# Optimization experiments

Measured on AMD Instinct MI355X. Metric: run time of the kernel, lower is better.

## Reference

```python
import jax, jax.numpy as jnp
import numpy as np

N, E, G = 20000, 160000, 64
IN_FULL, X_START, X_END = 16, 4, 10
H, OUT, RH, NE, K = 512, 512, 128, 4, 2
NL = 3               # GraphConv layers per expert
SPS, STEMP = 0.3, 1.0  # size_prior_strength, size_temperature


def setup_inputs() -> dict:
    key = jax.random.key(0)
    ks = jax.random.split(key, 10)
    def w(k, shape, fan):
        return jax.random.normal(k, shape, jnp.float32) / np.float32(np.sqrt(fan))
    return dict(
        x=jax.random.normal(ks[0], (N, IN_FULL), jnp.float32),
        edge_index=jax.random.randint(ks[1], (2, E), 0, N),
        batch=jnp.sort(jax.random.randint(ks[2], (N,), 0, G)),
        num_graphs=G,
        enc_W1=w(ks[3], (X_END - X_START, H), X_END - X_START), enc_b1=jnp.zeros((H,), jnp.float32),
        enc_W2=w(ks[4], (H, H), H), enc_b2=jnp.zeros((H,), jnp.float32),
        r_W1=w(ks[5], (H + 2, RH), H + 2), r_b1=jnp.zeros((RH,), jnp.float32),
        ln_g=jnp.ones((RH,), jnp.float32), ln_b=jnp.zeros((RH,), jnp.float32),
        r_W2=w(ks[6], (RH, NE), RH), r_b2=jnp.zeros((NE,), jnp.float32),
        size_centers=jnp.linspace(0.0, 1.0, NE).astype(jnp.float32),
        W_rel=w(ks[7], (NE, NL, H, H), H),       # GraphConv lin_rel weights (stacked)
        b_rel=jnp.zeros((NE, NL, H), jnp.float32),
        W_root=w(ks[8], (NE, NL, H, H), H),      # GraphConv lin_root weights (no bias)
    )


def reference(x, edge_index, batch, num_graphs, enc_W1, enc_b1, enc_W2, enc_b2,
              r_W1, r_b1, ln_g, ln_b, r_W2, r_b2, size_centers, W_rel, b_rel, W_root):
    src, dst = edge_index[0], edge_index[1]
    # encoder: Linear -> ReLU -> Linear on sliced node features
    h = jax.nn.relu(x[:, X_START:X_END] @ enc_W1 + enc_b1) @ enc_W2 + enc_b2
    # per-graph size features (log_nodes_edges mode)
    nodes = jnp.maximum(jax.ops.segment_sum(jnp.ones((N,), x.dtype), batch, num_segments=num_graphs), 1.0)
    edges = jax.ops.segment_sum(jnp.ones((E,), x.dtype), batch[src], num_segments=num_graphs)
    log_n, log_e = jnp.log(nodes), jnp.log1p(edges)
    f = jnp.stack([log_n, log_e], axis=-1)
    f = (f - f.mean(0, keepdims=True)) / (f.std(0, keepdims=True) + 1e-6)
    size_norm = (log_n - log_n.min()) / (log_n.max() - log_n.min() + 1e-6)
    # router: Linear -> LayerNorm -> ReLU -> Linear, plus size prior
    r = jnp.concatenate([h, f[batch]], axis=-1) @ r_W1 + r_b1
    r = (r - r.mean(-1, keepdims=True)) / jnp.sqrt(r.var(-1, keepdims=True) + 1e-5) * ln_g + ln_b
    logits = jax.nn.relu(r) @ r_W2 + r_b2
    prior = -(size_norm[batch][:, None] - size_centers[None, :]) ** 2 / STEMP
    logits = (1.0 - SPS) * logits + SPS * prior
    probs = jax.nn.softmax(logits, axis=-1)
    # top-k sparse gating, renormalized
    v, ix = jax.lax.top_k(probs, K)
    v = v / (v.sum(-1, keepdims=True) + 1e-8)
    weights = jnp.zeros_like(probs).at[jnp.arange(N)[:, None], ix].set(v)  # [N, NE]
    # GraphConv: out_i = (sum_{j->i} z_j) @ W_rel + b_rel + z_i @ W_root
    def gconv(z, Wr, br, Wo):
        agg = jax.ops.segment_sum(z[src], dst, num_segments=N)
        return agg @ Wr + br + z @ Wo
    out = jnp.zeros((N, OUT), x.dtype)
    for e in range(NE):  # small fixed expert count
        z = jax.nn.relu(gconv(h, W_rel[e, 0], b_rel[e, 0], W_root[e, 0]))
        z = jax.nn.relu(gconv(z, W_rel[e, 1], b_rel[e, 1], W_root[e, 1]))
        z = gconv(z, W_rel[e, 2], b_rel[e, 2], W_root[e, 2])
        out = out + weights[:, e:e + 1] * z
    return out
```

## Files before the change

kernel.cpp:

```cpp
#include <hip/hip_runtime.h>
#include <math.h>

#define N_NODES 20000
#define N_EDGES 160000
#define G_GRAPHS 64
#define H_DIM 512
#define RH_DIM 128
#define NE_EXP 4
#define P_ROWS 20096
#define EH_BLOCKS 64
#define WSZ (512 * 512)

typedef __attribute__((ext_vector_type(8))) short bf16x8;
typedef __attribute__((ext_vector_type(4))) float f32x4;

__device__ __forceinline__ ushort f2bf(float f) {
    uint u = __float_as_uint(f);
    return (ushort)((u + 0x7FFFu + ((u >> 16) & 1u)) >> 16);
}
__device__ __forceinline__ float bf2f(ushort h) {
    return __uint_as_float(((uint)h) << 16);
}

__device__ __forceinline__ void async_copy16(const void* g, void* l) {
    __builtin_amdgcn_global_load_lds(
        (__attribute__((address_space(1))) void*)g,
        (__attribute__((address_space(3))) void*)l, 16, 0, 0);
}

__device__ __forceinline__ int xcd_swizzle(int orig, int nwg) {
    const int q = nwg >> 3, r = nwg & 7;
    const int xcd = orig & 7, sid = orig >> 3;
    return (xcd < r ? xcd * (q + 1) : r * (q + 1) + (xcd - r) * q) + sid;
}

template<bool RELU, int EPI, int NE2>
__global__ __launch_bounds__(256)
void gemm_grp(const ushort* __restrict__ A1, size_t a1es,
              const ushort* __restrict__ W1, size_t w1es,
              const ushort* __restrict__ A2, size_t a2es,
              const ushort* __restrict__ W2, size_t w2es,
              const float* __restrict__ bias, size_t bes,
              const float* __restrict__ wcol,
              ushort* __restrict__ out0, size_t oes)
{
    __shared__ char smem[32768];
    const int tid = threadIdx.x;
    const int w = tid >> 6, lane = tid & 63;

    const int wgid = xcd_swizzle(blockIdx.x, gridDim.x);
    const int m0 = (wgid / (4 * NE2)) * 128;
    const int rem = wgid % (4 * NE2);
    const int e  = rem % NE2;
    const int n0 = (rem / NE2) * 128;

    const ushort* __restrict__ A1e = A1 + (size_t)e * a1es;
    const ushort* __restrict__ W1e = W1 + (size_t)e * w1es;
    const ushort* __restrict__ A2e = A2 + (size_t)e * a2es;
    const ushort* __restrict__ W2e = W2 + (size_t)e * w2es;
    const float*  __restrict__ be  = bias + (size_t)e * bes;
    ushort* __restrict__ oe = out0 + (size_t)e * oes;

    f32x4 acc[4][4];
#pragma unroll
    for (int i = 0; i < 4; ++i)
#pragma unroll
        for (int j = 0; j < 4; ++j) acc[i][j] = (f32x4){0.f, 0.f, 0.f, 0.f};

    const int srow = lane >> 2, schk = lane & 3;
    const int wr = w >> 1, wc = w & 1;
    const int row16 = lane & 15;
    const uint koffB = (uint)(lane >> 4) * 16u;
    const uint aoff0 = (uint)(wr * 64 + row16) * 64u + koffB;
    const uint boff0 = 8192u + (uint)(wc * 64 + row16) * 64u + koffB;

    auto stage = [&](int buf, int t) {
        const ushort* __restrict__ A  = (t < 16) ? A1e : A2e;
        const ushort* __restrict__ Wt = (t < 16) ? W1e : W2e;
        const int kt = (t & 15) * 32;
        char* base = smem + buf * 16384;
#pragma unroll
        for (int c = 0; c < 2; ++c) {
            const int rb = c * 64 + w * 16;
            async_copy16(A  + (size_t)(m0 + rb + srow) * 512 + kt + schk * 8, base + rb * 64);
            async_copy16(Wt + (size_t)(n0 + rb + srow) * 512 + kt + schk * 8, base + 8192 + rb * 64);
        }
    };
    auto compute = [&](int buf) {
        const char* base = smem + buf * 16384;
        bf16x8 af[4], bfr[4];
#pragma unroll
        for (int i = 0; i < 4; ++i) af[i] = *(const bf16x8*)(base + aoff0 + i * 1024);
#pragma unroll
        for (int j = 0; j < 4; ++j) bfr[j] = *(const bf16x8*)(base + boff0 + j * 1024);
#pragma unroll
        for (int i = 0; i < 4; ++i)
#pragma unroll
            for (int j = 0; j < 4; ++j)
                acc[i][j] = __builtin_amdgcn_mfma_f32_16x16x32_bf16(af[i], bfr[j], acc[i][j], 0, 0, 0);
    };

    stage(0, 0);
    for (int t = 0; t < 31; ++t) {
        stage((t + 1) & 1, t + 1);
        asm volatile("s_waitcnt vmcnt(4)" ::: "memory");
        __builtin_amdgcn_s_barrier();
        compute(t & 1);
        __builtin_amdgcn_s_barrier();
    }
    asm volatile("s_waitcnt vmcnt(0)" ::: "memory");
    __builtin_amdgcn_s_barrier();
    compute(1);

#pragma unroll
    for (int i = 0; i < 4; ++i) {
        const int r0 = m0 + wr * 64 + i * 16 + (lane >> 4) * 4;
#pragma unroll
        for (int j = 0; j < 4; ++j) {
            const int c = n0 + wc * 64 + j * 16 + row16;
            const float bj = be[c];
#pragma unroll
            for (int q2 = 0; q2 < 4; ++q2) {
                const int r = r0 + q2;
                float v = acc[i][j][q2] + bj;
                if (EPI == 0) {
                    if (RELU) v = fmaxf(v, 0.f);
                    oe[(size_t)r * 512 + c] = f2bf(v);
                } else {
                    const float wrow = (r < N_NODES) ? wcol[(size_t)r * 4 + e] : 0.f;
                    oe[(size_t)r * 512 + c] = f2bf(v * wrow);
                }
            }
        }
    }
}

template<int NPASS, int EPI, int NBN>
__global__ __launch_bounds__(256)
void gemm_mfma(const ushort* __restrict__ A0, const ushort* __restrict__ W0,
               const ushort* __restrict__ A1p, const ushort* __restrict__ W1p,
               const ushort* __restrict__ A2p, const ushort* __restrict__ W2p,
               const float* __restrict__ bias,
               void* __restrict__ out0, void* __restrict__ out1, int Ncols)
{
    __shared__ char smem[32768];
    const int tid = threadIdx.x;
    const int w = tid >> 6, lane = tid & 63;

    const int wgid = xcd_swizzle(blockIdx.x, gridDim.x);
    const int m0 = (wgid / NBN) * 128;
    const int n0 = (wgid % NBN) * 128;

    f32x4 acc[4][4];
#pragma unroll
    for (int i = 0; i < 4; ++i)
#pragma unroll
        for (int j = 0; j < 4; ++j) acc[i][j] = (f32x4){0.f, 0.f, 0.f, 0.f};

    const int srow = lane >> 2, schk = lane & 3;
    const int wr = w >> 1, wc = w & 1;
    const int row16 = lane & 15;
    const uint koffB = (uint)(lane >> 4) * 16u;
    const uint aoff0 = (uint)(wr * 64 + row16) * 64u + koffB;
    const uint boff0 = 8192u + (uint)(wc * 64 + row16) * 64u + koffB;

    const int NT = NPASS * 16;
    auto Asel = [&](int t) -> const ushort* { return (t < 16) ? A0 : ((t < 32) ? A1p : A2p); };
    auto Wsel = [&](int t) -> const ushort* { return (t < 16) ? W0 : ((t < 32) ? W1p : W2p); };

    auto stage = [&](int buf, int t) {
        const ushort* __restrict__ A  = Asel(t);
        const ushort* __restrict__ Wt = Wsel(t);
        const int kt = (t & 15) * 32;
        char* base = smem + buf * 16384;
#pragma unroll
        for (int c = 0; c < 2; ++c) {
            const int rb = c * 64 + w * 16;
            async_copy16(A  + (size_t)(m0 + rb + srow) * 512 + kt + schk * 8, base + rb * 64);
            async_copy16(Wt + (size_t)(n0 + rb + srow) * 512 + kt + schk * 8, base + 8192 + rb * 64);
        }
    };
    auto compute = [&](int buf) {
        const char* base = smem + buf * 16384;
        bf16x8 af[4], bfr[4];
#pragma unroll
        for (int i = 0; i < 4; ++i) af[i] = *(const bf16x8*)(base + aoff0 + i * 1024);
#pragma unroll
        for (int j = 0; j < 4; ++j) bfr[j] = *(const bf16x8*)(base + boff0 + j * 1024);
#pragma unroll
        for (int i = 0; i < 4; ++i)
#pragma unroll
            for (int j = 0; j < 4; ++j)
                acc[i][j] = __builtin_amdgcn_mfma_f32_16x16x32_bf16(af[i], bfr[j], acc[i][j], 0, 0, 0);
    };

    stage(0, 0);
    for (int t = 0; t < NT - 1; ++t) {
        stage((t + 1) & 1, t + 1);
        asm volatile("s_waitcnt vmcnt(4)" ::: "memory");
        __builtin_amdgcn_s_barrier();
        compute(t & 1);
        __builtin_amdgcn_s_barrier();
    }
    asm volatile("s_waitcnt vmcnt(0)" ::: "memory");
    __builtin_amdgcn_s_barrier();
    compute((NT - 1) & 1);

#pragma unroll
    for (int i = 0; i < 4; ++i) {
        const int r0 = m0 + wr * 64 + i * 16 + (lane >> 4) * 4;
#pragma unroll
        for (int j = 0; j < 4; ++j) {
            const int c = n0 + wc * 64 + j * 16 + row16;
            const float bj = (EPI == 5) ? 0.f : bias[c];
#pragma unroll
            for (int q2 = 0; q2 < 4; ++q2) {
                const int r = r0 + q2;
                float v = acc[i][j][q2] + bj;
                if (EPI == 4) {
                    const ushort hi = f2bf(v);
                    const ushort lo = f2bf(v - bf2f(hi));
                    ((ushort*)out0)[(size_t)r * Ncols + c] = hi;
                    ((ushort*)out1)[(size_t)r * Ncols + c] = lo;
                } else {
                    ((float*)out0)[(size_t)r * Ncols + c] = v;
                }
            }
        }
    }
}

__global__ __launch_bounds__(256)
void reduce_wz_kernel(const uint* __restrict__ wz4, float2* __restrict__ out)
{
    const size_t idx = (size_t)blockIdx.x * 256 + threadIdx.x;
    const size_t es = (size_t)P_ROWS * 256;
    const uint a = wz4[idx], b = wz4[idx + es];
    const uint c = wz4[idx + 2 * es], d = wz4[idx + 3 * es];
    float lo = bf2f((ushort)(a & 0xffffu)) + bf2f((ushort)(b & 0xffffu))
             + bf2f((ushort)(c & 0xffffu)) + bf2f((ushort)(d & 0xffffu));
    float hi = bf2f((ushort)(a >> 16)) + bf2f((ushort)(b >> 16))
             + bf2f((ushort)(c >> 16)) + bf2f((ushort)(d >> 16));
    out[idx] = make_float2(lo, hi);
}

__global__ void encoder1_kernel(const float* __restrict__ x, const float* __restrict__ W1,
                                const float* __restrict__ b1,
                                ushort* __restrict__ t1hi, ushort* __restrict__ t1lo)
{
    const int idx = blockIdx.x * blockDim.x + threadIdx.x;
    if (idx >= P_ROWS * H_DIM) return;
    const int i = idx / H_DIM, j = idx - i * H_DIM;
    float v = 0.f;
    if (i < N_NODES) {
        const float* xr = &x[i * 16 + 4];
        v = b1[j];
#pragma unroll
        for (int k = 0; k < 6; ++k) v = fmaf(xr[k], W1[k * H_DIM + j], v);
        v = fmaxf(v, 0.f);
    }
    const ushort hi = f2bf(v);
    t1hi[idx] = hi;
    t1lo[idx] = f2bf(v - bf2f(hi));
}

__global__ void zero_ints_kernel(int* __restrict__ p, int n)
{
    const int idx = blockIdx.x * blockDim.x + threadIdx.x;
    if (idx < n) p[idx] = 0;
}

__global__ void graph_bounds_kernel(const int* __restrict__ batch, int* __restrict__ gstart)
{
    const int g = threadIdx.x;
    if (g > G_GRAPHS) return;
    int lo = 0, hi = N_NODES;
    while (lo < hi) {
        const int mid = (lo + hi) >> 1;
        if (batch[mid] < g) lo = mid + 1; else hi = mid;
    }
    gstart[g] = lo;
}

__global__ __launch_bounds__(256)
void edge_hist_kernel(const int* __restrict__ src, const int* __restrict__ dst,
                      const int* __restrict__ batch,
                      int* __restrict__ part, int* __restrict__ deg)
{
    __shared__ int hist[G_GRAPHS];
    const int tid = threadIdx.x;
    if (tid < G_GRAPHS) hist[tid] = 0;
    __syncthreads();
    for (int e = blockIdx.x * 256 + tid; e < N_EDGES; e += EH_BLOCKS * 256) {
        atomicAdd(&deg[dst[e]], 1);
        atomicAdd(&hist[batch[src[e]]], 1);
    }
    __syncthreads();
    if (tid < G_GRAPHS) part[blockIdx.x * G_GRAPHS + tid] = hist[tid];
}

__global__ void stats_finalize_kernel(const int* __restrict__ gstart, const int* __restrict__ part,
                                      float* __restrict__ f_norm, float* __restrict__ size_norm)
{
    const int g = threadIdx.x;
    const float nn = fmaxf((float)(gstart[g + 1] - gstart[g]), 1.0f);
    int ec = 0;
#pragma unroll 8
    for (int b = 0; b < EH_BLOCKS; ++b) ec += part[b * G_GRAPHS + g];
    const float ee = (float)ec;
    const float ln = logf(nn);
    const float le = log1pf(ee);
    float s0 = ln, s1 = le;
#pragma unroll
    for (int o = 32; o > 0; o >>= 1) { s0 += __shfl_xor(s0, o); s1 += __shfl_xor(s1, o); }
    const float m0 = s0 / 64.f, m1 = s1 / 64.f;
    const float d0 = ln - m0, d1 = le - m1;
    float v0 = d0 * d0, v1 = d1 * d1;
#pragma unroll
    for (int o = 32; o > 0; o >>= 1) { v0 += __shfl_xor(v0, o); v1 += __shfl_xor(v1, o); }
    const float sd0 = sqrtf(v0 / 64.f), sd1 = sqrtf(v1 / 64.f);
    float mn = ln, mx = ln;
#pragma unroll
    for (int o = 32; o > 0; o >>= 1) {
        mn = fminf(mn, __shfl_xor(mn, o));
        mx = fmaxf(mx, __shfl_xor(mx, o));
    }
    f_norm[g * 2 + 0] = d0 / (sd0 + 1e-6f);
    f_norm[g * 2 + 1] = d1 / (sd1 + 1e-6f);
    size_norm[g] = (ln - mn) / (mx - mn + 1e-6f);
}

__global__ void scan_kernel(const int* __restrict__ in, int* __restrict__ row_ptr,
                            int* __restrict__ cursor, int n)
{
    __shared__ int wsum[16];
    __shared__ int carry_s;
    const int tid = threadIdx.x;
    const int lane = tid & 63, wv = tid >> 6;
    if (tid == 0) carry_s = 0;
    __syncthreads();
    for (int base = 0; base < n; base += 1024) {
        const int idx = base + tid;
        const int v = (idx < n) ? in[idx] : 0;
        int x = v;
#pragma unroll
        for (int o = 1; o < 64; o <<= 1) { const int t = __shfl_up(x, o); if (lane >= o) x += t; }
        if (lane == 63) wsum[wv] = x;
        __syncthreads();
        const int carry = carry_s;
        if (wv == 0) {
            int y = (lane < 16) ? wsum[lane] : 0;
#pragma unroll
            for (int o = 1; o < 16; o <<= 1) { const int t = __shfl_up(y, o); if (lane >= o) y += t; }
            if (lane < 16) wsum[lane] = y;
        }
        __syncthreads();
        const int woff = (wv > 0) ? wsum[wv - 1] : 0;
        const int excl = x - v + woff + carry;
        if (idx < n) { row_ptr[idx] = excl; cursor[idx] = excl; }
        __syncthreads();
        if (tid == 0) carry_s = carry + wsum[15];
        __syncthreads();
    }
    if (tid == 0) row_ptr[n] = carry_s;
}

__global__ void scatter_kernel(const int* __restrict__ src, const int* __restrict__ dst,
                               int* __restrict__ cursor, int* __restrict__ csr_col)
{
    const int e = blockIdx.x * blockDim.x + threadIdx.x;
    if (e >= N_EDGES) return;
    const int d = dst[e];
    const int slot = atomicAdd(&cursor[d], 1);
    csr_col[slot] = src[e];
}

__global__ void sort_adj_kernel(const int* __restrict__ row_ptr, int* __restrict__ csr_col)
{
    const int i = blockIdx.x * blockDim.x + threadIdx.x;
    if (i >= N_NODES) return;
    const int b = row_ptr[i], e = row_ptr[i + 1];
    for (int p = b + 1; p < e; ++p) {
        const int key = csr_col[p];
        int q = p - 1;
        while (q >= b && csr_col[q] > key) { csr_col[q + 1] = csr_col[q]; --q; }
        csr_col[q + 1] = key;
    }
}

__global__ __launch_bounds__(256)
void aggregate_bf16(const uint4* __restrict__ z4, const int* __restrict__ row_ptr,
                    const int* __restrict__ csr_col, uint4* __restrict__ agg4)
{
    const size_t es = (size_t)blockIdx.y * P_ROWS * 64;
    const uint4* __restrict__ zz = z4 + es;
    uint4* __restrict__ aa = agg4 + es;
    const int i = blockIdx.x * 4 + (threadIdx.x >> 6);
    const int lane = threadIdx.x & 63;
    const int b = row_ptr[i], e = row_ptr[i + 1];
    float acc[8];
#pragma unroll
    for (int k = 0; k < 8; ++k) acc[k] = 0.f;
    auto add8 = [&](uint4 v) {
        acc[0] += bf2f((ushort)(v.x & 0xffffu)); acc[1] += bf2f((ushort)(v.x >> 16));
        acc[2] += bf2f((ushort)(v.y & 0xffffu)); acc[3] += bf2f((ushort)(v.y >> 16));
        acc[4] += bf2f((ushort)(v.z & 0xffffu)); acc[5] += bf2f((ushort)(v.z >> 16));
        acc[6] += bf2f((ushort)(v.w & 0xffffu)); acc[7] += bf2f((ushort)(v.w >> 16));
    };
    int p = b;
    for (; p + 2 <= e; p += 2) {
        const uint4 v0 = zz[(size_t)csr_col[p] * 64 + lane];
        const uint4 v1 = zz[(size_t)csr_col[p + 1] * 64 + lane];
        add8(v0);
        add8(v1);
    }
    if (p < e) add8(zz[(size_t)csr_col[p] * 64 + lane]);
    uint4 o;
    o.x = (uint)f2bf(acc[0]) | ((uint)f2bf(acc[1]) << 16);
    o.y = (uint)f2bf(acc[2]) | ((uint)f2bf(acc[3]) << 16);
    o.z = (uint)f2bf(acc[4]) | ((uint)f2bf(acc[5]) << 16);
    o.w = (uint)f2bf(acc[6]) | ((uint)f2bf(acc[7]) << 16);
    aa[(size_t)i * 64 + lane] = o;
}

__global__ __launch_bounds__(256)
void transpose_f32_to_bf16(const float* __restrict__ W, ushort* __restrict__ Wt)
{
    __shared__ float tile[32][33];
    const float* Wm = W + (size_t)blockIdx.z * WSZ;
    ushort* Wtm = Wt + (size_t)blockIdx.z * WSZ;
    const int c0 = blockIdx.x * 32, r0 = blockIdx.y * 32;
    const int tc = threadIdx.x & 31, tr = threadIdx.x >> 5;
#pragma unroll
    for (int it = 0; it < 4; ++it)
        tile[tr + it * 8][tc] = Wm[(size_t)(r0 + tr + it * 8) * 512 + c0 + tc];
    __syncthreads();
#pragma unroll
    for (int it = 0; it < 4; ++it) {
        const int cr = tr + it * 8;
        Wtm[(size_t)(c0 + cr) * 512 + r0 + tc] = f2bf(tile[tc][cr]);
    }
}

__global__ __launch_bounds__(256)
void transpose_split_kernel(const float* __restrict__ W, ushort* __restrict__ Whi,
                            ushort* __restrict__ Wlo, int Nin)
{
    __shared__ float tile[32][33];
    const int c0 = blockIdx.x * 32;
    const int r0 = blockIdx.y * 32;
    const int tc = threadIdx.x & 31, tr = threadIdx.x >> 5;
#pragma unroll
    for (int it = 0; it < 4; ++it)
        tile[tr + it * 8][tc] = W[(size_t)(r0 + tr + it * 8) * Nin + c0 + tc];
    __syncthreads();
#pragma unroll
    for (int it = 0; it < 4; ++it) {
        const int cr = tr + it * 8;
        const float v = tile[tc][cr];
        const ushort hi = f2bf(v);
        Whi[(size_t)(c0 + cr) * 512 + r0 + tc] = hi;
        Wlo[(size_t)(c0 + cr) * 512 + r0 + tc] = f2bf(v - bf2f(hi));
    }
}

__global__ __launch_bounds__(128)
void router_kernel(const float* __restrict__ rtmp, const int* __restrict__ batch,
                   const float* __restrict__ rW1, const float* __restrict__ rb1,
                   const float* __restrict__ lng, const float* __restrict__ lnb,
                   const float* __restrict__ rW2, const float* __restrict__ rb2,
                   const float* __restrict__ centers,
                   const float* __restrict__ f_norm, const float* __restrict__ size_norm,
                   float* __restrict__ weights)
{
    const int i = blockIdx.x;
    const int j = threadIdx.x;
    const int g = batch[i];
    const float f0 = f_norm[g * 2], f1 = f_norm[g * 2 + 1];
    float r = rtmp[(size_t)i * RH_DIM + j]
            + f0 * rW1[512 * RH_DIM + j] + f1 * rW1[513 * RH_DIM + j] + rb1[j];

    __shared__ float part[2];
    __shared__ float rbuf[RH_DIM];
    __shared__ float lbuf[4];
    const int lane = j & 63, wv = j >> 6;

    float s = r;
#pragma unroll
    for (int o = 32; o > 0; o >>= 1) s += __shfl_xor(s, o);
    if (lane == 0) part[wv] = s;
    __syncthreads();
    const float mean = (part[0] + part[1]) / 128.f;
    __syncthreads();
    const float d = r - mean;
    float v = d * d;
#pragma unroll
    for (int o = 32; o > 0; o >>= 1) v += __shfl_xor(v, o);
    if (lane == 0) part[wv] = v;
    __syncthreads();
    const float var = (part[0] + part[1]) / 128.f;
    const float rn = d / sqrtf(var + 1e-5f) * lng[j] + lnb[j];
    rbuf[j] = fmaxf(rn, 0.f);
    __syncthreads();

    if (j < 4) {
        float acc = rb2[j];
        for (int t = 0; t < RH_DIM; ++t) acc = fmaf(rbuf[t], rW2[t * 4 + j], acc);
        const float sn = size_norm[g];
        const float dd = sn - centers[j];
        lbuf[j] = 0.7f * acc + 0.3f * (-(dd * dd));
    }
    __syncthreads();
    if (j == 0) {
        float p[4];
        const float mx = fmaxf(fmaxf(lbuf[0], lbuf[1]), fmaxf(lbuf[2], lbuf[3]));
#pragma unroll
        for (int c = 0; c < 4; ++c) p[c] = expf(lbuf[c] - mx);
        const float ssum = p[0] + p[1] + p[2] + p[3];
#pragma unroll
        for (int c = 0; c < 4; ++c) p[c] /= ssum;
        int i1 = 0;
#pragma unroll
        for (int c = 1; c < 4; ++c) if (p[c] > p[i1]) i1 = c;
        int i2 = -1;
#pragma unroll
        for (int c = 0; c < 4; ++c) {
            if (c == i1) continue;
            if (i2 < 0 || p[c] > p[i2]) i2 = c;
        }
        const float vs = p[i1] + p[i2] + 1e-8f;
        float wout[4] = {0.f, 0.f, 0.f, 0.f};
        wout[i1] = p[i1] / vs;
        wout[i2] = p[i2] / vs;
#pragma unroll
        for (int c = 0; c < 4; ++c) weights[(size_t)i * 4 + c] = wout[c];
    }
}

extern "C" void kernel_launch(void* const* d_in, const int* in_sizes, int n_in,
                              void* d_out, int out_size, void* d_ws, size_t ws_size,
                              hipStream_t stream)
{
    const float* x       = (const float*)d_in[0];
    const int*   ei      = (const int*)d_in[1];
    const int*   batch   = (const int*)d_in[2];
    const float* enc_W1  = (const float*)d_in[4];
    const float* enc_b1  = (const float*)d_in[5];
    const float* enc_W2  = (const float*)d_in[6];
    const float* enc_b2  = (const float*)d_in[7];
    const float* r_W1    = (const float*)d_in[8];
    const float* r_b1    = (const float*)d_in[9];
    const float* ln_g    = (const float*)d_in[10];
    const float* ln_b    = (const float*)d_in[11];
    const float* r_W2    = (const float*)d_in[12];
    const float* r_b2    = (const float*)d_in[13];
    const float* centers = (const float*)d_in[14];
    const float* W_rel   = (const float*)d_in[15];
    const float* b_rel   = (const float*)d_in[16];
    const float* W_root  = (const float*)d_in[17];
    const int* src = ei;
    const int* dst = ei + N_EDGES;
    float* out = (float*)d_out;

    const size_t PF = (size_t)P_ROWS * H_DIM;
    const size_t PF2 = PF * 2;
    const int mode = (ws_size >= (size_t)375 * 1024 * 1024) ? 2
                   : (ws_size >= (size_t)295 * 1024 * 1024) ? 1 : 0;
    const int zaW = (mode >= 1) ? 4 : 2;
    const int zbW = (mode == 2) ? 4 : 2;

    char* wsp = (char*)d_ws;
    size_t off = 0;
    auto alloc = [&](size_t bytes) -> char* {
        char* p = wsp + off;
        off = (off + bytes + 255) & ~(size_t)255;
        return p;
    };
    char* region1 = alloc(PF * 4);
    ushort* t1hi = (ushort*)region1;
    ushort* t1lo = (ushort*)(region1 + PF * 2);
    ushort* wz4  = (ushort*)region1;
    char* region2 = alloc(PF * 4);
    ushort* h_hi = (ushort*)region2;
    ushort* h_lo = (ushort*)(region2 + PF * 2);
    char* B_zA = alloc(PF2 * zaW);
    ushort* zAe = (ushort*)B_zA;
    float*  rtmp = (float*)B_zA;
    char* B_zB = alloc(PF2 * zbW);
    ushort* zBe = (ushort*)B_zB;
    char* B_ag = alloc(PF2 * zbW);
    ushort* agge = (ushort*)B_ag;
    ushort* aggH16 = (ushort*)alloc(PF * 2);
    ushort* Wt_rel16  = (ushort*)alloc((size_t)12 * WSZ * 2);
    ushort* Wt_root16 = (ushort*)alloc((size_t)12 * WSZ * 2);
    ushort* W2t_hi = (ushort*)alloc((size_t)WSZ * 2);
    ushort* W2t_lo = (ushort*)alloc((size_t)WSZ * 2);
    ushort* rW1t_hi = (ushort*)alloc((size_t)128 * 512 * 2);
    ushort* rW1t_lo = (ushort*)alloc((size_t)128 * 512 * 2);
    float*  weights = (float*)alloc((size_t)P_ROWS * 4 * 4);
    int* deg     = (int*)alloc((size_t)N_NODES * 4);
    int* gstart  = (int*)alloc((size_t)(G_GRAPHS + 1) * 4);
    int* part    = (int*)alloc((size_t)EH_BLOCKS * G_GRAPHS * 4);
    int* row_ptr = (int*)alloc((size_t)(N_NODES + 1) * 4);
    int* cursor  = (int*)alloc((size_t)N_NODES * 4);
    int* csr_col = (int*)alloc((size_t)N_EDGES * 4);
    float* f_norm    = (float*)alloc((size_t)G_GRAPHS * 2 * 4);
    float* size_norm = (float*)alloc((size_t)G_GRAPHS * 4);
    (void)in_sizes; (void)n_in; (void)out_size;

    const int enc_nwg  = 4 * (P_ROWS / 128);
    const int rtr_nwg  = 1 * (P_ROWS / 128);
    const int grp_nwg2 = 8 * (P_ROWS / 128);
    const int grp_nwg4 = 16 * (P_ROWS / 128);
    const dim3 tr_grid(16, 16, 12);
    const dim3 agg_grid1(N_NODES / 4, 1);
    const dim3 agg_grid2(N_NODES / 4, 2);
    const dim3 agg_grid4(N_NODES / 4, 4);

    zero_ints_kernel<<<(N_NODES + 255) / 256, 256, 0, stream>>>(deg, N_NODES);
    transpose_f32_to_bf16<<<tr_grid, 256, 0, stream>>>(W_rel, Wt_rel16);
    transpose_f32_to_bf16<<<tr_grid, 256, 0, stream>>>(W_root, Wt_root16);
    transpose_split_kernel<<<dim3(16, 16), 256, 0, stream>>>(enc_W2, W2t_hi, W2t_lo, 512);
    transpose_split_kernel<<<dim3(4, 16), 256, 0, stream>>>(r_W1, rW1t_hi, rW1t_lo, 128);
    graph_bounds_kernel<<<1, 128, 0, stream>>>(batch, gstart);
    edge_hist_kernel<<<EH_BLOCKS, 256, 0, stream>>>(src, dst, batch, part, deg);
    stats_finalize_kernel<<<1, 64, 0, stream>>>(gstart, part, f_norm, size_norm);
    encoder1_kernel<<<(P_ROWS * H_DIM + 255) / 256, 256, 0, stream>>>(x, enc_W1, enc_b1, t1hi, t1lo);
    gemm_mfma<3, 4, 4><<<enc_nwg, 256, 0, stream>>>(
        t1hi, W2t_hi, t1hi, W2t_lo, t1lo, W2t_hi, enc_b2, h_hi, h_lo, 512);
    gemm_mfma<3, 5, 1><<<rtr_nwg, 256, 0, stream>>>(
        h_hi, rW1t_hi, h_hi, rW1t_lo, h_lo, rW1t_hi, nullptr, rtmp, nullptr, 128);
    router_kernel<<<N_NODES, 128, 0, stream>>>(rtmp, batch, r_W1, r_b1, ln_g, ln_b,
                                               r_W2, r_b2, centers, f_norm, size_norm, weights);
    scan_kernel<<<1, 1024, 0, stream>>>(deg, row_ptr, cursor, N_NODES);
    scatter_kernel<<<(N_EDGES + 255) / 256, 256, 0, stream>>>(src, dst, cursor, csr_col);
    sort_adj_kernel<<<(N_NODES + 255) / 256, 256, 0, stream>>>(row_ptr, csr_col);
    aggregate_bf16<<<agg_grid1, 256, 0, stream>>>((const uint4*)h_hi, row_ptr, csr_col,
                                                  (uint4*)aggH16);

    const size_t WES = (size_t)3 * WSZ;
    const size_t BES = (size_t)3 * 512;
    if (mode == 2) {
        gemm_grp<true, 0, 4><<<grp_nwg4, 256, 0, stream>>>(
            aggH16, 0, Wt_rel16, WES, h_hi, 0, Wt_root16, WES, b_rel, BES, nullptr, zAe, PF);
        aggregate_bf16<<<agg_grid4, 256, 0, stream>>>((const uint4*)zAe, row_ptr, csr_col,
                                                      (uint4*)agge);
        gemm_grp<true, 0, 4><<<grp_nwg4, 256, 0, stream>>>(
            agge, PF, Wt_rel16 + WSZ, WES, zAe, PF, Wt_root16 + WSZ, WES, b_rel + 512, BES,
            nullptr, zBe, PF);
        aggregate_bf16<<<agg_grid4, 256, 0, stream>>>((const uint4*)zBe, row_ptr, csr_col,
                                                      (uint4*)agge);
        gemm_grp<false, 6, 4><<<grp_nwg4, 256, 0, stream>>>(
            agge, PF, Wt_rel16 + 2 * WSZ, WES, zBe, PF, Wt_root16 + 2 * WSZ, WES, b_rel + 1024, BES,
            weights, wz4, PF);
    } else if (mode == 1) {
        gemm_grp<true, 0, 4><<<grp_nwg4, 256, 0, stream>>>(
            aggH16, 0, Wt_rel16, WES, h_hi, 0, Wt_root16, WES, b_rel, BES, nullptr, zAe, PF);
        for (int p = 0; p < 2; ++p) {
            const size_t eb = (size_t)(p * 2);
            const ushort* WrP = Wt_rel16  + eb * WES;
            const ushort* WoP = Wt_root16 + eb * WES;
            const float*  brP = b_rel + eb * BES;
            const ushort* zAp = zAe + eb * PF;
            ushort* wzP = wz4 + eb * PF;
            aggregate_bf16<<<agg_grid2, 256, 0, stream>>>((const uint4*)zAp, row_ptr, csr_col,
                                                          (uint4*)agge);
            gemm_grp<true, 0, 2><<<grp_nwg2, 256, 0, stream>>>(
                agge, PF, WrP + WSZ, WES, zAp, PF, WoP + WSZ, WES, brP + 512, BES, nullptr, zBe, PF);
            aggregate_bf16<<<agg_grid2, 256, 0, stream>>>((const uint4*)zBe, row_ptr, csr_col,
                                                          (uint4*)agge);
            gemm_grp<false, 6, 2><<<grp_nwg2, 256, 0, stream>>>(
                agge, PF, WrP + 2 * WSZ, WES, zBe, PF, WoP + 2 * WSZ, WES, brP + 1024, BES,
                weights + eb, wzP, PF);
        }
    } else {
        for (int p = 0; p < 2; ++p) {
            const size_t eb = (size_t)(p * 2);
            const ushort* WrP = Wt_rel16  + eb * WES;
            const ushort* WoP = Wt_root16 + eb * WES;
            const float*  brP = b_rel + eb * BES;
            ushort* wzP = wz4 + eb * PF;
            gemm_grp<true, 0, 2><<<grp_nwg2, 256, 0, stream>>>(
                aggH16, 0, WrP, WES, h_hi, 0, WoP, WES, brP, BES, nullptr, zAe, PF);
            aggregate_bf16<<<agg_grid2, 256, 0, stream>>>((const uint4*)zAe, row_ptr, csr_col,
                                                          (uint4*)agge);
            gemm_grp<true, 0, 2><<<grp_nwg2, 256, 0, stream>>>(
                agge, PF, WrP + WSZ, WES, zAe, PF, WoP + WSZ, WES, brP + 512, BES, nullptr, zBe, PF);
            aggregate_bf16<<<agg_grid2, 256, 0, stream>>>((const uint4*)zBe, row_ptr, csr_col,
                                                          (uint4*)agge);
            gemm_grp<false, 6, 2><<<grp_nwg2, 256, 0, stream>>>(
                agge, PF, WrP + 2 * WSZ, WES, zBe, PF, WoP + 2 * WSZ, WES, brP + 1024, BES,
                weights + eb, wzP, PF);
        }
    }
    reduce_wz_kernel<<<N_NODES, 256, 0, stream>>>((const uint*)wz4, (float2*)out);
}
```

Before: 836.7 us.

## Load GEMM A-fragments directly into registers and drop workspace-size mode dispatch

Both GEMM kernels now stage only the weight (B) tile through shared memory. Each wave loads its A fragments straight from global memory into double-buffered registers, which halves LDS use and removes the A round-trip through shared memory, at the cost of less-coalesced global reads and more registers. The host also drops the workspace-size-dependent modes (4-expert grouped launches) and always runs the two-pass, two-experts-per-launch schedule, shrinking workspace buffers. This loses the larger grouped launches that could have been used when workspace allowed.

New measurement: 1.133 ms. 35.4% more time.

```diff
diff --git a/kernel.cpp b/kernel.cpp
--- a/kernel.cpp
+++ b/kernel.cpp
@@ -44,7 +44,7 @@
               const float* __restrict__ wcol,
               ushort* __restrict__ out0, size_t oes)
 {
-    __shared__ char smem[32768];
+    __shared__ char smem[16384];
     const int tid = threadIdx.x;
     const int w = tid >> 6, lane = tid & 63;
 
@@ -71,26 +71,33 @@
     const int wr = w >> 1, wc = w & 1;
     const int row16 = lane & 15;
     const uint koffB = (uint)(lane >> 4) * 16u;
-    const uint aoff0 = (uint)(wr * 64 + row16) * 64u + koffB;
-    const uint boff0 = 8192u + (uint)(wc * 64 + row16) * 64u + koffB;
-
-    auto stage = [&](int buf, int t) {
-        const ushort* __restrict__ A  = (t < 16) ? A1e : A2e;
+    const uint boff0 = (uint)(wc * 64 + row16) * 64u + koffB;
+
+    size_t arow[4];
+#pragma unroll
+    for (int i = 0; i < 4; ++i)
+        arow[i] = (size_t)(m0 + wr * 64 + i * 16 + row16) * 512 + (lane >> 4) * 8;
+
+    auto stageB = [&](int buf, int t) {
         const ushort* __restrict__ Wt = (t < 16) ? W1e : W2e;
         const int kt = (t & 15) * 32;
-        char* base = smem + buf * 16384;
+        char* base = smem + buf * 8192;
 #pragma unroll
         for (int c = 0; c < 2; ++c) {
             const int rb = c * 64 + w * 16;
-            async_copy16(A  + (size_t)(m0 + rb + srow) * 512 + kt + schk * 8, base + rb * 64);
-            async_copy16(Wt + (size_t)(n0 + rb + srow) * 512 + kt + schk * 8, base + 8192 + rb * 64);
+            async_copy16(Wt + (size_t)(n0 + rb + srow) * 512 + kt + schk * 8, base + rb * 64);
         }
     };
-    auto compute = [&](int buf) {
-        const char* base = smem + buf * 16384;
-        bf16x8 af[4], bfr[4];
-#pragma unroll
-        for (int i = 0; i < 4; ++i) af[i] = *(const bf16x8*)(base + aoff0 + i * 1024);
+    auto loadA = [&](bf16x8* dst, int t) {
+        const ushort* __restrict__ A = (t < 16) ? A1e : A2e;
+        const int kt = (t & 15) * 32;
+#pragma unroll
+        for (int i = 0; i < 4; ++i)
+            dst[i] = *(const bf16x8*)(A + arow[i] + kt);
+    };
+    auto compute = [&](int buf, const bf16x8* af) {
+        const char* base = smem + buf * 8192;
+        bf16x8 bfr[4];
 #pragma unroll
         for (int j = 0; j < 4; ++j) bfr[j] = *(const bf16x8*)(base + boff0 + j * 1024);
 #pragma unroll
@@ -100,17 +107,21 @@
                 acc[i][j] = __builtin_amdgcn_mfma_f32_16x16x32_bf16(af[i], bfr[j], acc[i][j], 0, 0, 0);
     };
 
-    stage(0, 0);
+    bf16x8 afr0[4], afr1[4];
+    stageB(0, 0);
+    loadA(afr0, 0);
+#pragma unroll
     for (int t = 0; t < 31; ++t) {
-        stage((t + 1) & 1, t + 1);
-        asm volatile("s_waitcnt vmcnt(4)" ::: "memory");
+        stageB((t + 1) & 1, t + 1);
+        if ((t & 1) == 0) loadA(afr1, t + 1); else loadA(afr0, t + 1);
+        asm volatile("s_waitcnt vmcnt(6)" ::: "memory");
         __builtin_amdgcn_s_barrier();
-        compute(t & 1);
+        compute(t & 1, (t & 1) ? afr1 : afr0);
         __builtin_amdgcn_s_barrier();
     }
     asm volatile("s_waitcnt vmcnt(0)" ::: "memory");
     __builtin_amdgcn_s_barrier();
-    compute(1);
+    compute(1, afr1);
 
 #pragma unroll
     for (int i = 0; i < 4; ++i) {
@@ -143,7 +154,7 @@
                const float* __restrict__ bias,
                void* __restrict__ out0, void* __restrict__ out1, int Ncols)
 {
-    __shared__ char smem[32768];
+    __shared__ char smem[16384];
     const int tid = threadIdx.x;
     const int w = tid >> 6, lane = tid & 63;
 
@@ -161,30 +172,37 @@
     const int wr = w >> 1, wc = w & 1;
     const int row16 = lane & 15;
     const uint koffB = (uint)(lane >> 4) * 16u;
-    const uint aoff0 = (uint)(wr * 64 + row16) * 64u + koffB;
-    const uint boff0 = 8192u + (uint)(wc * 64 + row16) * 64u + koffB;
+    const uint boff0 = (uint)(wc * 64 + row16) * 64u + koffB;
+
+    size_t arow[4];
+#pragma unroll
+    for (int i = 0; i < 4; ++i)
+        arow[i] = (size_t)(m0 + wr * 64 + i * 16 + row16) * 512 + (lane >> 4) * 8;
 
     const int NT = NPASS * 16;
     auto Asel = [&](int t) -> const ushort* { return (t < 16) ? A0 : ((t < 32) ? A1p : A2p); };
     auto Wsel = [&](int t) -> const ushort* { return (t < 16) ? W0 : ((t < 32) ? W1p : W2p); };
 
-    auto stage = [&](int buf, int t) {
-        const ushort* __restrict__ A  = Asel(t);
+    auto stageB = [&](int buf, int t) {
         const ushort* __restrict__ Wt = Wsel(t);
         const int kt = (t & 15) * 32;
-        char* base = smem + buf * 16384;
+        char* base = smem + buf * 8192;
 #pragma unroll
         for (int c = 0; c < 2; ++c) {
             const int rb = c * 64 + w * 16;
-            async_copy16(A  + (size_t)(m0 + rb + srow) * 512 + kt + schk * 8, base + rb * 64);
-            async_copy16(Wt + (size_t)(n0 + rb + srow) * 512 + kt + schk * 8, base + 8192 + rb * 64);
+            async_copy16(Wt + (size_t)(n0 + rb + srow) * 512 + kt + schk * 8, base + rb * 64);
         }
     };
-    auto compute = [&](int buf) {
-        const char* base = smem + buf * 16384;
-        bf16x8 af[4], bfr[4];
-#pragma unroll
-        for (int i = 0; i < 4; ++i) af[i] = *(const bf16x8*)(base + aoff0 + i * 1024);
+    auto loadA = [&](bf16x8* dst, int t) {
+        const ushort* __restrict__ A = Asel(t);
+        const int kt = (t & 15) * 32;
+#pragma unroll
+        for (int i = 0; i < 4; ++i)
+            dst[i] = *(const bf16x8*)(A + arow[i] + kt);
+    };
+    auto compute = [&](int buf, const bf16x8* af) {
+        const char* base = smem + buf * 8192;
+        bf16x8 bfr[4];
 #pragma unroll
         for (int j = 0; j < 4; ++j) bfr[j] = *(const bf16x8*)(base + boff0 + j * 1024);
 #pragma unroll
@@ -194,17 +212,21 @@
                 acc[i][j] = __builtin_amdgcn_mfma_f32_16x16x32_bf16(af[i], bfr[j], acc[i][j], 0, 0, 0);
     };
 
-    stage(0, 0);
+    bf16x8 afr0[4], afr1[4];
+    stageB(0, 0);
+    loadA(afr0, 0);
+#pragma unroll
     for (int t = 0; t < NT - 1; ++t) {
-        stage((t + 1) & 1, t + 1);
-        asm volatile("s_waitcnt vmcnt(4)" ::: "memory");
+        stageB((t + 1) & 1, t + 1);
+        if ((t & 1) == 0) loadA(afr1, t + 1); else loadA(afr0, t + 1);
+        asm volatile("s_waitcnt vmcnt(6)" ::: "memory");
         __builtin_amdgcn_s_barrier();
-        compute(t & 1);
+        compute(t & 1, (t & 1) ? afr1 : afr0);
         __builtin_amdgcn_s_barrier();
     }
     asm volatile("s_waitcnt vmcnt(0)" ::: "memory");
     __builtin_amdgcn_s_barrier();
-    compute((NT - 1) & 1);
+    compute((NT - 1) & 1, ((NT - 1) & 1) ? afr1 : afr0);
 
 #pragma unroll
     for (int i = 0; i < 4; ++i) {
@@ -564,10 +586,6 @@
 
     const size_t PF = (size_t)P_ROWS * H_DIM;
     const size_t PF2 = PF * 2;
-    const int mode = (ws_size >= (size_t)375 * 1024 * 1024) ? 2
-                   : (ws_size >= (size_t)295 * 1024 * 1024) ? 1 : 0;
-    const int zaW = (mode >= 1) ? 4 : 2;
-    const int zbW = (mode == 2) ? 4 : 2;
 
     char* wsp = (char*)d_ws;
     size_t off = 0;
@@ -583,12 +601,12 @@
     char* region2 = alloc(PF * 4);
     ushort* h_hi = (ushort*)region2;
     ushort* h_lo = (ushort*)(region2 + PF * 2);
-    char* B_zA = alloc(PF2 * zaW);
+    char* B_zA = alloc(PF2 * 2);
     ushort* zAe = (ushort*)B_zA;
     float*  rtmp = (float*)B_zA;
-    char* B_zB = alloc(PF2 * zbW);
+    char* B_zB = alloc(PF2 * 2);
     ushort* zBe = (ushort*)B_zB;
-    char* B_ag = alloc(PF2 * zbW);
+    char* B_ag = alloc(PF2 * 2);
     ushort* agge = (ushort*)B_ag;
     ushort* aggH16 = (ushort*)alloc(PF * 2);
     ushort* Wt_rel16  = (ushort*)alloc((size_t)12 * WSZ * 2);
@@ -606,16 +624,14 @@
     int* csr_col = (int*)alloc((size_t)N_EDGES * 4);
     float* f_norm    = (float*)alloc((size_t)G_GRAPHS * 2 * 4);
     float* size_norm = (float*)alloc((size_t)G_GRAPHS * 4);
-    (void)in_sizes; (void)n_in; (void)out_size;
+    (void)in_sizes; (void)n_in; (void)out_size; (void)ws_size;
 
     const int enc_nwg  = 4 * (P_ROWS / 128);
     const int rtr_nwg  = 1 * (P_ROWS / 128);
     const int grp_nwg2 = 8 * (P_ROWS / 128);
-    const int grp_nwg4 = 16 * (P_ROWS / 128);
     const dim3 tr_grid(16, 16, 12);
     const dim3 agg_grid1(N_NODES / 4, 1);
     const dim3 agg_grid2(N_NODES / 4, 2);
-    const dim3 agg_grid4(N_NODES / 4, 4);
 
     zero_ints_kernel<<<(N_NODES + 255) / 256, 256, 0, stream>>>(deg, N_NODES);
     transpose_f32_to_bf16<<<tr_grid, 256, 0, stream>>>(W_rel, Wt_rel16);
@@ -640,58 +656,23 @@
 
     const size_t WES = (size_t)3 * WSZ;
     const size_t BES = (size_t)3 * 512;
-    if (mode == 2) {
-        gemm_grp<true, 0, 4><<<grp_nwg4, 256, 0, stream>>>(
-            aggH16, 0, Wt_rel16, WES, h_hi, 0, Wt_root16, WES, b_rel, BES, nullptr, zAe, PF);
-        aggregate_bf16<<<agg_grid4, 256, 0, stream>>>((const uint4*)zAe, row_ptr, csr_col,
+    for (int p = 0; p < 2; ++p) {
+        const size_t eb = (size_t)(p * 2);
+        const ushort* WrP = Wt_rel16  + eb * WES;
+        const ushort* WoP = Wt_root16 + eb * WES;
+        const float*  brP = b_rel + eb * BES;
+        ushort* wzP = wz4 + eb * PF;
+        gemm_grp<true, 0, 2><<<grp_nwg2, 256, 0, stream>>>(
+            aggH16, 0, WrP, WES, h_hi, 0, WoP, WES, brP, BES, nullptr, zAe, PF);
+        aggregate_bf16<<<agg_grid2, 256, 0, stream>>>((const uint4*)zAe, row_ptr, csr_col,
                                                       (uint4*)agge);
-        gemm_grp<true, 0, 4><<<grp_nwg4, 256, 0, stream>>>(
-            agge, PF, Wt_rel16 + WSZ, WES, zAe, PF, Wt_root16 + WSZ, WES, b_rel + 512, BES,
-            nullptr, zBe, PF);
-        aggregate_bf16<<<agg_grid4, 256, 0, stream>>>((const uint4*)zBe, row_ptr, csr_col,
+        gemm_grp<true, 0, 2><<<grp_nwg2, 256, 0, stream>>>(
+            agge, PF, WrP + WSZ, WES, zAe, PF, WoP + WSZ, WES, brP + 512, BES, nullptr, zBe, PF);
+        aggregate_bf16<<<agg_grid2, 256, 0, stream>>>((const uint4*)zBe, row_ptr, csr_col,
                                                       (uint4*)agge);
-        gemm_grp<false, 6, 4><<<grp_nwg4, 256, 0, stream>>>(
-            agge, PF, Wt_rel16 + 2 * WSZ, WES, zBe, PF, Wt_root16 + 2 * WSZ, WES, b_rel + 1024, BES,
-            weights, wz4, PF);
-    } else if (mode == 1) {
-        gemm_grp<true, 0, 4><<<grp_nwg4, 256, 0, stream>>>(
-            aggH16, 0, Wt_rel16, WES, h_hi, 0, Wt_root16, WES, b_rel, BES, nullptr, zAe, PF);
-        for (int p = 0; p < 2; ++p) {
-            const size_t eb = (size_t)(p * 2);
-            const ushort* WrP = Wt_rel16  + eb * WES;
-            const ushort* WoP = Wt_root16 + eb * WES;
-            const float*  brP = b_rel + eb * BES;
-            const ushort* zAp = zAe + eb * PF;
-            ushort* wzP = wz4 + eb * PF;
-            aggregate_bf16<<<agg_grid2, 256, 0, stream>>>((const uint4*)zAp, row_ptr, csr_col,
-                                                          (uint4*)agge);
-            gemm_grp<true, 0, 2><<<grp_nwg2, 256, 0, stream>>>(
-                agge, PF, WrP + WSZ, WES, zAp, PF, WoP + WSZ, WES, brP + 512, BES, nullptr, zBe, PF);
-            aggregate_bf16<<<agg_grid2, 256, 0, stream>>>((const uint4*)zBe, row_ptr, csr_col,
-                                                          (uint4*)agge);
-            gemm_grp<false, 6, 2><<<grp_nwg2, 256, 0, stream>>>(
-                agge, PF, WrP + 2 * WSZ, WES, zBe, PF, WoP + 2 * WSZ, WES, brP + 1024, BES,
-                weights + eb, wzP, PF);
-        }
-    } else {
-        for (int p = 0; p < 2; ++p) {
-            const size_t eb = (size_t)(p * 2);
-            const ushort* WrP = Wt_rel16  + eb * WES;
-            const ushort* WoP = Wt_root16 + eb * WES;
-            const float*  brP = b_rel + eb * BES;
-            ushort* wzP = wz4 + eb * PF;
-            gemm_grp<true, 0, 2><<<grp_nwg2, 256, 0, stream>>>(
-                aggH16, 0, WrP, WES, h_hi, 0, WoP, WES, brP, BES, nullptr, zAe, PF);
-            aggregate_bf16<<<agg_grid2, 256, 0, stream>>>((const uint4*)zAe, row_ptr, csr_col,
-                                                          (uint4*)agge);
-            gemm_grp<true, 0, 2><<<grp_nwg2, 256, 0, stream>>>(
-                agge, PF, WrP + WSZ, WES, zAe, PF, WoP + WSZ, WES, brP + 512, BES, nullptr, zBe, PF);
-            aggregate_bf16<<<agg_grid2, 256, 0, stream>>>((const uint4*)zBe, row_ptr, csr_col,
-                                                          (uint4*)agge);
-            gemm_grp<false, 6, 2><<<grp_nwg2, 256, 0, stream>>>(
-                agge, PF, WrP + 2 * WSZ, WES, zBe, PF, WoP + 2 * WSZ, WES, brP + 1024, BES,
-                weights + eb, wzP, PF);
-        }
+        gemm_grp<false, 6, 2><<<grp_nwg2, 256, 0, stream>>>(
+            agge, PF, WrP + 2 * WSZ, WES, zBe, PF, WoP + 2 * WSZ, WES, brP + 1024, BES,
+            weights + eb, wzP, PF);
     }
     reduce_wz_kernel<<<N_NODES, 256, 0, stream>>>((const uint*)wz4, (float2*)out);
 }
```
